# Performance work log

Measured on AMD Instinct MI355X. Metric: run time of the kernel, lower is better.

The kernel has to match this reference:

```python
import jax, jax.numpy as jnp
import numpy as np

B, T, F, H, L = 16384, 24, 7, 8, 4
DENSE = [T * H, 1024, 2048, 4]


def setup_inputs() -> dict:
    key = jax.random.key(0)
    d = {"x": jax.random.normal(jax.random.fold_in(key, 0), (B, T, F), jnp.float32)}
    k = 1
    s = 1.0 / np.sqrt(H)  # torch LSTM init bound
    for l in range(L):
        in_dim = F if l == 0 else H
        for name, shape in [("Wih", (4 * H, in_dim)), ("Whh", (4 * H, H)), ("bih", (4 * H,)), ("bhh", (4 * H,))]:
            d[f"{name}{l}"] = jax.random.uniform(jax.random.fold_in(key, k), shape, jnp.float32, -s, s)
            k += 1
    for i in range(1, len(DENSE)):
        si = 1.0 / np.sqrt(DENSE[i - 1])
        d[f"Wd{i}"] = jax.random.uniform(jax.random.fold_in(key, k), (DENSE[i], DENSE[i - 1]), jnp.float32, -si, si)
        k += 1
        d[f"bd{i}"] = jax.random.uniform(jax.random.fold_in(key, k), (DENSE[i],), jnp.float32, -si, si)
        k += 1
    return d


def _lstm_layer(xs, Wih, Whh, b):
    # xs: [T, B, in] -> ys: [T, B, H]; torch gate order i,f,g,o
    Hn = Whh.shape[1]
    h0 = jnp.zeros((xs.shape[1], Hn), xs.dtype)

    def step(carry, xt):
        h, c = carry
        z = xt @ Wih.T + h @ Whh.T + b  # [B, 4H]
        i, f, g, o = jnp.split(z, 4, axis=-1)
        c = jax.nn.sigmoid(f) * c + jax.nn.sigmoid(i) * jnp.tanh(g)
        h = jax.nn.sigmoid(o) * jnp.tanh(c)
        return (h, c), h

    (_, _), ys = jax.lax.scan(step, (h0, h0), xs)
    return ys


def _forward(x, lstm_params, dense_params):
    xs = jnp.transpose(x, (1, 0, 2))  # [T, B, F]
    for (Wih, Whh, bih, bhh) in lstm_params:
        xs = _lstm_layer(xs, Wih, Whh, bih + bhh)
    out = jnp.transpose(xs, (1, 0, 2)).reshape(x.shape[0], T * H)  # [B, 192]
    (W1, b1), (W2, b2), (W3, b3) = dense_params
    out = jax.nn.relu(out @ W1.T + b1)
    out = jax.nn.relu(out @ W2.T + b2)
    return out @ W3.T + b3  # [B, num_classes]


def reference(x, Wih0, Whh0, bih0, bhh0, Wih1, Whh1, bih1, bhh1, Wih2, Whh2, bih2, bhh2, Wih3, Whh3, bih3, bhh3, Wd1, bd1, Wd2, bd2, Wd3, bd3):
    lstm_params = [(Wih0, Whh0, bih0, bhh0), (Wih1, Whh1, bih1, bhh1), (Wih2, Whh2, bih2, bhh2), (Wih3, Whh3, bih3, bhh3)]
    dense_params = [(Wd1, bd1), (Wd2, bd2), (Wd3, bd3)]
    return _forward(x, lstm_params, dense_params)
```

## Files before the change

### kernel.cpp

```cpp
#include <hip/hip_runtime.h>
#include <hip/hip_bf16.h>

typedef __attribute__((ext_vector_type(4))) float f32x4;
typedef __attribute__((ext_vector_type(16))) float f32x16;
typedef __attribute__((ext_vector_type(2))) float f32x2;
typedef __attribute__((ext_vector_type(8))) short bf16x8;

__device__ __forceinline__ ushort f2bf(float f) {
    union { float f; uint u; } v; v.f = f;
    uint u = v.u;
    return (ushort)((u + 0x7fffu + ((u >> 16) & 1u)) >> 16);
}
__device__ __forceinline__ float sigm(float x) {
    return __builtin_amdgcn_rcpf(1.0f + __builtin_amdgcn_exp2f(x * -1.442695040888963f));
}
__device__ __forceinline__ float tanh_(float x) {
    return 2.0f * __builtin_amdgcn_rcpf(1.0f + __builtin_amdgcn_exp2f(x * -2.885390081777927f)) - 1.0f;
}

typedef const __attribute__((address_space(1))) unsigned int ga_u32;
typedef __attribute__((address_space(3))) unsigned int lds_u32;
__device__ __forceinline__ void g2l16(const void* g, void* l) {
    __builtin_amdgcn_global_load_lds((ga_u32*)(unsigned long long)g,
                                     (lds_u32*)(unsigned int)(unsigned long long)l,
                                     16, 0, 0);
}

struct LstmW {
    const float* wih[4];
    const float* whh[4];
    const float* bih[4];
    const float* bhh[4];
};

__device__ __forceinline__ void gates8p(const f32x2 w01[8], const f32x2 w23[8],
                                        const float xv8[8], f32x2& a01, f32x2& a23) {
#pragma unroll
    for (int k = 0; k < 8; ++k) {
        f32x2 xv = {xv8[k], xv8[k]};
        a01 += w01[k] * xv;
        a23 += w23[k] * xv;
    }
}
__device__ __forceinline__ void cellup(f32x2 a01, f32x2 a23, float& h, float& c) {
    c = sigm(a01.y) * c + sigm(a01.x) * tanh_(a23.x);
    h = sigm(a23.y) * tanh_(c);
}
__device__ __forceinline__ void ld8(const float* p, float v[8]) {
    float4 a = *(const float4*)p;
    float4 b = *(const float4*)(p + 4);
    v[0] = a.x; v[1] = a.y; v[2] = a.z; v[3] = a.w;
    v[4] = b.x; v[5] = b.y; v[6] = b.z; v[7] = b.w;
}

__global__ __launch_bounds__(256) void pre_kernel(const float* __restrict__ x, LstmW p,
                                                  ushort* __restrict__ Y,
                                                  const float* __restrict__ W1,
                                                  const float* __restrict__ W2,
                                                  ushort* __restrict__ W1b,
                                                  ushort* __restrict__ W2b,
                                                  const float* __restrict__ b3,
                                                  float* __restrict__ out) {
    __shared__ float xs[32 * 168];
    __shared__ float hb[32 * 200];

    const int tid = threadIdx.x;
    if (blockIdx.x >= 512) {
        const int tg = (blockIdx.x - 512) * 256 + tid;
        if (tg < 16384) {
            float4 bv = {b3[0], b3[1], b3[2], b3[3]};
            ((float4*)out)[tg] = bv;
        }
#pragma unroll
        for (int s = 0; s < 4; ++s) {
            int i = tg + s * 143360;
            const float4* src; ushort4* dst; int off;
            if (i < 49152) { src = (const float4*)W1; dst = (ushort4*)W1b; off = i; }
            else { src = (const float4*)W2; dst = (ushort4*)W2b; off = i - 49152; }
            float4 v = src[off];
            ushort4 r; r.x = f2bf(v.x); r.y = f2bf(v.y); r.z = f2bf(v.z); r.w = f2bf(v.w);
            dst[off] = r;
        }
        return;
    }

    const int e0 = blockIdx.x * 32;
    {
        const float4* s = (const float4*)(x + (size_t)e0 * 168);
        float4* d = (float4*)xs;
        for (int i = tid; i < 1344; i += 256) d[i] = s[i];
    }
    __syncthreads();

    const int el = tid >> 3, j = tid & 7;
    float* hr = hb + el * 200;
    const float* xr = xs + el * 168;

    f32x2 wx01[8], wx23[8], wh01[8], wh23[8], b01, b23;

    {
        const float* Wih = p.wih[0];
        const float* Whh = p.whh[0];
#pragma unroll
        for (int k = 0; k < 7; ++k) {
            wx01[k] = {Wih[(0 + j) * 7 + k], Wih[(8 + j) * 7 + k]};
            wx23[k] = {Wih[(16 + j) * 7 + k], Wih[(24 + j) * 7 + k]};
        }
#pragma unroll
        for (int k = 0; k < 8; ++k) {
            wh01[k] = {Whh[(0 + j) * 8 + k], Whh[(8 + j) * 8 + k]};
            wh23[k] = {Whh[(16 + j) * 8 + k], Whh[(24 + j) * 8 + k]};
        }
        b01 = {p.bih[0][j] + p.bhh[0][j], p.bih[0][8 + j] + p.bhh[0][8 + j]};
        b23 = {p.bih[0][16 + j] + p.bhh[0][16 + j], p.bih[0][24 + j] + p.bhh[0][24 + j]};

        float h = 0.f, c = 0.f;
        {
            f32x2 a01 = b01, a23 = b23;
#pragma unroll
            for (int k = 0; k < 7; ++k) {
                f32x2 xv = {xr[k], xr[k]};
                a01 += wx01[k] * xv; a23 += wx23[k] * xv;
            }
            cellup(a01, a23, h, c);
            hr[j] = h;
        }
        for (int t = 1; t < 24; ++t) {
            f32x2 a01 = b01, a23 = b23;
#pragma unroll
            for (int k = 0; k < 7; ++k) {
                f32x2 xv = {xr[t * 7 + k], xr[t * 7 + k]};
                a01 += wx01[k] * xv; a23 += wx23[k] * xv;
            }
            float hp[8]; ld8(&hr[(t - 1) * 8], hp);
            gates8p(wh01, wh23, hp, a01, a23);
            cellup(a01, a23, h, c);
            hr[t * 8 + j] = h;
        }
    }

#pragma unroll
    for (int l = 1; l < 4; ++l) {
        const float* Wih = p.wih[l];
        const float* Whh = p.whh[l];
#pragma unroll
        for (int k = 0; k < 8; ++k) {
            wx01[k] = {Wih[(0 + j) * 8 + k], Wih[(8 + j) * 8 + k]};
            wx23[k] = {Wih[(16 + j) * 8 + k], Wih[(24 + j) * 8 + k]};
            wh01[k] = {Whh[(0 + j) * 8 + k], Whh[(8 + j) * 8 + k]};
            wh23[k] = {Whh[(16 + j) * 8 + k], Whh[(24 + j) * 8 + k]};
        }
        b01 = {p.bih[l][j] + p.bhh[l][j], p.bih[l][8 + j] + p.bhh[l][8 + j]};
        b23 = {p.bih[l][16 + j] + p.bhh[l][16 + j], p.bih[l][24 + j] + p.bhh[l][24 + j]};

        float h = 0.f, c = 0.f;
        {
            float xin[8]; ld8(&hr[0], xin);
            f32x2 a01 = b01, a23 = b23;
            gates8p(wx01, wx23, xin, a01, a23);
            cellup(a01, a23, h, c);
            hr[j] = h;
            if (l == 3) Y[((size_t)(e0 + el) * 24) * 8 + j] = f2bf(h);
        }
        for (int t = 1; t < 24; ++t) {
            float xin[8]; ld8(&hr[t * 8], xin);
            float hp[8];  ld8(&hr[(t - 1) * 8], hp);
            f32x2 a01 = b01, a23 = b23;
            gates8p(wx01, wx23, xin, a01, a23);
            gates8p(wh01, wh23, hp, a01, a23);
            cellup(a01, a23, h, c);
            hr[t * 8 + j] = h;
            if (l == 3) Y[((size_t)(e0 + el) * 24 + t) * 8 + j] = f2bf(h);
        }
    }
}

template <int KDIM>
__device__ __forceinline__ void gemm_body(const ushort* __restrict__ A,
                                          const ushort* __restrict__ W,
                                          const float* __restrict__ bias,
                                          ushort* __restrict__ Hout, int N) {
    __shared__ alignas(16) ushort smem[16384];
    ushort* As = smem;
    ushort* Ws = smem + 8192;

    const int tid = threadIdx.x;
    const int m0 = blockIdx.x * 128;
    const int n0 = blockIdx.y * 128;
    const int lane = tid & 63;
    const int wv = tid >> 6;
    const int wm = (wv & 1) * 64;
    const int wn = (wv >> 1) * 64;
    const int l31 = lane & 31;
    const int kh = lane >> 5;

    const int lrow = lane >> 3;
    const int lchunk = (lane & 7) ^ lrow;
    const ushort* Ag = A + (size_t)(m0 + wv * 32 + lrow) * KDIM + lchunk * 8;
    const ushort* Wg = W + (size_t)(n0 + wv * 32 + lrow) * KDIM + lchunk * 8;
    ushort* Ald = As + wv * 2048;
    ushort* Wld = Ws + wv * 2048;

    const int r7 = l31 & 7;
    const int arow0 = (wm + l31) * 64;
    const int brow0 = (wn + l31) * 64;

    f32x16 acc[2][2];
#pragma unroll
    for (int mi = 0; mi < 2; ++mi)
#pragma unroll
        for (int ni = 0; ni < 2; ++ni)
#pragma unroll
            for (int r = 0; r < 16; ++r) acc[mi][ni][r] = 0.f;

    for (int k0 = 0; k0 < KDIM; k0 += 64) {
#pragma unroll
        for (int c = 0; c < 4; ++c)
            g2l16(Ag + (size_t)c * 8 * KDIM + k0, Ald + c * 512);
#pragma unroll
        for (int c = 0; c < 4; ++c)
            g2l16(Wg + (size_t)c * 8 * KDIM + k0, Wld + c * 512);
        __syncthreads();

#pragma unroll
        for (int ks = 0; ks < 4; ++ks) {
            const int ck = ((ks * 2 + kh) ^ r7) * 8;
            bf16x8 afr[2], bfr[2];
#pragma unroll
            for (int mi = 0; mi < 2; ++mi)
                afr[mi] = *(const bf16x8*)&As[arow0 + mi * 2048 + ck];
#pragma unroll
            for (int ni = 0; ni < 2; ++ni)
                bfr[ni] = *(const bf16x8*)&Ws[brow0 + ni * 2048 + ck];
#pragma unroll
            for (int mi = 0; mi < 2; ++mi)
#pragma unroll
                for (int ni = 0; ni < 2; ++ni)
                    acc[mi][ni] = __builtin_amdgcn_mfma_f32_32x32x16_bf16(afr[mi], bfr[ni],
                                                                         acc[mi][ni], 0, 0, 0);
        }
        __syncthreads();
    }

#pragma unroll
    for (int ni = 0; ni < 2; ++ni) {
        const int col = n0 + wn + ni * 32 + l31;
        const float b = bias[col];
#pragma unroll
        for (int mi = 0; mi < 2; ++mi)
#pragma unroll
            for (int r = 0; r < 16; ++r) {
                const int row = m0 + wm + mi * 32 + (r & 3) + 8 * (r >> 2) + 4 * kh;
                Hout[(size_t)row * N + col] = f2bf(fmaxf(acc[mi][ni][r] + b, 0.f));
            }
    }
}

__global__ __launch_bounds__(256, 4) void gemm1_kernel(const ushort* __restrict__ A,
                                                       const ushort* __restrict__ W,
                                                       const float* __restrict__ bias,
                                                       ushort* __restrict__ Hout, int N) {
    gemm_body<192>(A, W, bias, Hout, N);
}

template <int OFFB>
__device__ __forceinline__ bf16x8 dsr(unsigned a) {
    bf16x8 r;
    asm volatile("ds_read_b128 %0, %1 offset:%2"
                 : "=v"(r) : "v"(a), "i"(OFFB));
    return r;
}
template <int QA, int QB, int KS>
__device__ __forceinline__ void mma_sub(f32x4 acc[8][4], const bf16x8 afr[8],
                                        const bf16x8 br[4]) {
#pragma unroll
    for (int mi = 0; mi < 4; ++mi)
#pragma unroll
        for (int ni = 0; ni < 2; ++ni)
            acc[QA * 4 + mi][QB * 2 + ni] = __builtin_amdgcn_mfma_f32_16x16x32_bf16(
                afr[mi * 2 + KS], br[ni * 2 + KS], acc[QA * 4 + mi][QB * 2 + ni],
                0, 0, 0);
}

#define SBAR()  __builtin_amdgcn_s_barrier()
#define SCHED0() __builtin_amdgcn_sched_barrier(0)
#define LGKM(N) do { asm volatile("s_waitcnt lgkmcnt(" #N ")"); SCHED0(); } while (0)
#define VMC(N)  do { asm volatile("s_waitcnt vmcnt(" #N ")" ::: "memory"); } while (0)
#define PRIO1() __builtin_amdgcn_s_setprio(1)
#define PRIO0() do { __builtin_amdgcn_s_setprio(0); SCHED0(); } while (0)

__global__ __launch_bounds__(512) void gemm2_kernel(const ushort* __restrict__ A,
                                                    const ushort* __restrict__ W,
                                                    const float* __restrict__ bias,
                                                    const float* __restrict__ W3,
                                                    float* __restrict__ outf) {
    __shared__ alignas(16) ushort smem[65536];
    __shared__ alignas(16) float w3s[1040];

    const int tid = threadIdx.x;
    const int wg = ((int)blockIdx.x & 7) * 64 + ((int)blockIdx.x >> 3);
    const int m0 = (wg >> 3) << 8;
    const int n0 = (wg & 7) << 8;

    const int lane = tid & 63;
    const int wv = tid >> 6;

    const int lrow = tid >> 3;
    const int lc8 = ((tid & 7) ^ (lrow & 7)) << 3;
    const ushort* Ag = A + (size_t)(m0 + lrow) * 1024 + lc8;
    const ushort* Bg = W + (size_t)(n0 + lrow) * 1024 + lc8;
    ushort* const sA0 = smem;
    ushort* const sB0 = smem + 16384;
    ushort* const sA1 = smem + 32768;
    ushort* const sB1 = smem + 49152;
    const int srow64 = (wv << 3) * 64;

    const int l15 = lane & 15, kq = lane >> 4, r7 = l15 & 7;
    const int wM = wv >> 2, wN = wv & 3;
    const unsigned sbase = (unsigned)(unsigned long long)&smem[0];
    const unsigned pc0B = (unsigned)((kq ^ r7) << 4);
    const unsigned pc1B = pc0B ^ 64u;
    const unsigned aRowB = (unsigned)((wM * 128 + l15) * 128);
    const unsigned bRowB = (unsigned)((wN * 64 + l15) * 128);
    const unsigned aA0p0 = sbase + aRowB + pc0B;
    const unsigned aA0p1 = sbase + aRowB + pc1B;
    const unsigned aA1p0 = aA0p0 + 65536u;
    const unsigned aA1p1 = aA0p1 + 65536u;
    const unsigned bB0p0 = sbase + 32768u + bRowB + pc0B;
    const unsigned bB0p1 = sbase + 32768u + bRowB + pc1B;
    const unsigned bB1p0 = bB0p0 + 65536u;
    const unsigned bB1p1 = bB0p1 + 65536u;

    auto stA = [&](int buf, int h, int kt) {
        ushort* b = buf ? sA1 : sA0;
#pragma unroll
        for (int c = 0; c < 2; ++c)
            g2l16(Ag + (size_t)(h * 128 + c * 64) * 1024 + kt * 64,
                  b + (h * 128 + c * 64) * 64 + srow64);
    };
    auto stB = [&](int buf, int h, int kt) {
        ushort* b = buf ? sB1 : sB0;
#pragma unroll
        for (int c = 0; c < 2; ++c)
            g2l16(Bg + (size_t)(h * 128 + c * 64) * 1024 + kt * 64,
                  b + (h * 128 + c * 64) * 64 + srow64);
    };

    f32x4 acc[8][4];
#pragma unroll
    for (int i = 0; i < 8; ++i)
#pragma unroll
        for (int j = 0; j < 4; ++j)
#pragma unroll
            for (int r = 0; r < 4; ++r) acc[i][j][r] = 0.f;

#pragma unroll
    for (int i = 0; i < 2; ++i) {
        int idx = tid + i * 512;
        w3s[(idx >> 8) * 260 + (idx & 255)] = W3[(size_t)(idx >> 8) * 2048 + n0 + (idx & 255)];
    }
    float bias4[4];
#pragma unroll
    for (int ni = 0; ni < 4; ++ni) bias4[ni] = bias[n0 + wN * 64 + ni * 16 + l15];

    stA(0, 0, 0); stA(0, 1, 0); stB(0, 0, 0); stB(0, 1, 0);
    stB(1, 0, 1); stB(1, 1, 1); stA(1, 0, 1);
    asm volatile("s_waitcnt lgkmcnt(0)");
    VMC(6);
    SBAR(); SCHED0();

    bf16x8 afr[8], b0r[4], b1r[4];
    afr[0] = dsr<0>(aA0p0);    afr[2] = dsr<2048>(aA0p0);
    afr[4] = dsr<4096>(aA0p0); afr[6] = dsr<6144>(aA0p0);
    b0r[0] = dsr<0>(bB0p0);    b0r[2] = dsr<2048>(bB0p0);

#pragma unroll 1
    for (int it = 0; it < 8; ++it) {
        const int k1 = 2 * it + 1, k2 = 2 * it + 2, k3 = 2 * it + 3;
        const bool nl = (it < 7);
        SBAR(); SCHED0();
        afr[1] = dsr<0>(aA0p1);    afr[3] = dsr<2048>(aA0p1);
        afr[5] = dsr<4096>(aA0p1); afr[7] = dsr<6144>(aA0p1);
        b0r[1] = dsr<0>(bB0p1);    b0r[3] = dsr<2048>(bB0p1);
        stA(1, 1, k1);
        LGKM(6); PRIO1(); mma_sub<0, 0, 0>(acc, afr, b0r); PRIO0();
        b1r[0] = dsr<4096>(bB0p0); b1r[2] = dsr<6144>(bB0p0);
        LGKM(2); PRIO1(); mma_sub<0, 0, 1>(acc, afr, b0r); PRIO0();
        SBAR(); SCHED0();
        b1r[1] = dsr<4096>(bB0p1); b1r[3] = dsr<6144>(bB0p1);
        LGKM(2); PRIO1(); mma_sub<0, 1, 0>(acc, afr, b1r); PRIO0();
        afr[0] = dsr<8192>(aA0p0);  afr[2] = dsr<10240>(aA0p0);
        afr[4] = dsr<12288>(aA0p0); afr[6] = dsr<14336>(aA0p0);
        LGKM(4); PRIO1(); mma_sub<0, 1, 1>(acc, afr, b1r); PRIO0();
        SBAR(); SCHED0();
        afr[1] = dsr<8192>(aA0p1);  afr[3] = dsr<10240>(aA0p1);
        afr[5] = dsr<12288>(aA0p1); afr[7] = dsr<14336>(aA0p1);
        if (nl) stB(0, 0, k2);
        LGKM(4); PRIO1(); mma_sub<1, 1, 0>(acc, afr, b1r); PRIO0();
        LGKM(0); PRIO1(); mma_sub<1, 1, 1>(acc, afr, b1r); PRIO0();
        if (nl) { VMC(2); } else { VMC(0); }
        SBAR(); SCHED0();
        if (nl) { stB(0, 1, k2); stA(0, 0, k2); }
        PRIO1(); mma_sub<1, 0, 0>(acc, afr, b0r); PRIO0();
        afr[0] = dsr<8192>(aA1p0);  afr[2] = dsr<10240>(aA1p0);
        afr[4] = dsr<12288>(aA1p0); afr[6] = dsr<14336>(aA1p0);
        b0r[0] = dsr<0>(bB1p0);     b0r[2] = dsr<2048>(bB1p0);
        PRIO1(); mma_sub<1, 0, 1>(acc, afr, b0r); PRIO0();
        SBAR(); SCHED0();
        afr[1] = dsr<8192>(aA1p1);  afr[3] = dsr<10240>(aA1p1);
        afr[5] = dsr<12288>(aA1p1); afr[7] = dsr<14336>(aA1p1);
        b0r[1] = dsr<0>(bB1p1);     b0r[3] = dsr<2048>(bB1p1);
        if (nl) stA(0, 1, k2);
        LGKM(6); PRIO1(); mma_sub<1, 0, 0>(acc, afr, b0r); PRIO0();
        b1r[0] = dsr<4096>(bB1p0); b1r[2] = dsr<6144>(bB1p0);
        LGKM(2); PRIO1(); mma_sub<1, 0, 1>(acc, afr, b0r); PRIO0();
        SBAR(); SCHED0();
        b1r[1] = dsr<4096>(bB1p1); b1r[3] = dsr<6144>(bB1p1);
        LGKM(2); PRIO1(); mma_sub<1, 1, 0>(acc, afr, b1r); PRIO0();
        afr[0] = dsr<0>(aA1p0);    afr[2] = dsr<2048>(aA1p0);
        afr[4] = dsr<4096>(aA1p0); afr[6] = dsr<6144>(aA1p0);
        LGKM(4); PRIO1(); mma_sub<1, 1, 1>(acc, afr, b1r); PRIO0();
        SBAR(); SCHED0();
        afr[1] = dsr<0>(aA1p1);    afr[3] = dsr<2048>(aA1p1);
        afr[5] = dsr<4096>(aA1p1); afr[7] = dsr<6144>(aA1p1);
        if (nl) stB(1, 0, k3);
        LGKM(4); PRIO1(); mma_sub<0, 1, 0>(acc, afr, b1r); PRIO0();
        LGKM(0); PRIO1(); mma_sub<0, 1, 1>(acc, afr, b1r); PRIO0();
        if (nl) { VMC(2); }
        SBAR(); SCHED0();
        if (nl) { stB(1, 1, k3); stA(1, 0, k3); }
        PRIO1(); mma_sub<0, 0, 0>(acc, afr, b0r); PRIO0();
        if (nl) {
            afr[0] = dsr<0>(aA0p0);    afr[2] = dsr<2048>(aA0p0);
            afr[4] = dsr<4096>(aA0p0); afr[6] = dsr<6144>(aA0p0);
            b0r[0] = dsr<0>(bB0p0);    b0r[2] = dsr<2048>(bB0p0);
        }
        PRIO1(); mma_sub<0, 0, 1>(acc, afr, b0r); PRIO0();
    }

    float* Cs = (float*)smem;
    const int drow = tid >> 3;
    const int j8 = tid & 7;
    __syncthreads();
#pragma unroll
    for (int s = 0; s < 4; ++s) {
        if (wM == (s >> 1)) {
            const int mb = (s & 1) * 4;
#pragma unroll
            for (int mi = 0; mi < 4; ++mi)
#pragma unroll
                for (int ni = 0; ni < 4; ++ni) {
                    f32x4 v = acc[mb + mi][ni];
                    const int cbase = (mi * 16 + kq * 4) * 260 + wN * 64 + ni * 16 + l15;
#pragma unroll
                    for (int r = 0; r < 4; ++r)
                        Cs[cbase + r * 260] = fmaxf(v[r] + bias4[ni], 0.f);
                }
        }
        __syncthreads();
        {
            const float* crow = &Cs[drow * 260 + j8 * 4];
            f32x4 pp = {0.f, 0.f, 0.f, 0.f};
#pragma unroll
            for (int k = 0; k < 8; ++k) {
                f32x4 cv = *(const f32x4*)(crow + k * 32);
#pragma unroll
                for (int q = 0; q < 4; ++q) {
                    f32x4 wv4 = *(const f32x4*)(&w3s[q * 260 + j8 * 4 + k * 32]);
                    pp[q] += cv[0] * wv4[0] + cv[1] * wv4[1] + cv[2] * wv4[2] + cv[3] * wv4[3];
                }
            }
#pragma unroll
            for (int m = 1; m < 8; m <<= 1) {
#pragma unroll
                for (int q = 0; q < 4; ++q) pp[q] += __shfl_xor(pp[q], m);
            }
            const float pv = (j8 == 0) ? pp[0] : (j8 == 1) ? pp[1]
                           : (j8 == 2) ? pp[2] : pp[3];
            if (j8 < 4)
                atomicAdd(&outf[(size_t)(m0 + s * 64 + drow) * 4 + j8], pv);
        }
        __syncthreads();
    }
}

extern "C" void kernel_launch(void* const* d_in, const int* in_sizes, int n_in,
                              void* d_out, int out_size, void* d_ws, size_t ws_size,
                              hipStream_t stream) {
    const float* x = (const float*)d_in[0];
    LstmW w;
    for (int l = 0; l < 4; ++l) {
        w.wih[l] = (const float*)d_in[1 + 4 * l];
        w.whh[l] = (const float*)d_in[2 + 4 * l];
        w.bih[l] = (const float*)d_in[3 + 4 * l];
        w.bhh[l] = (const float*)d_in[4 + 4 * l];
    }
    const float* Wd1 = (const float*)d_in[17];
    const float* bd1 = (const float*)d_in[18];
    const float* Wd2 = (const float*)d_in[19];
    const float* bd2 = (const float*)d_in[20];
    const float* Wd3 = (const float*)d_in[21];
    const float* bd3 = (const float*)d_in[22];
    float* out = (float*)d_out;

    ushort* Y   = (ushort*)d_ws;
    ushort* H1  = (ushort*)((char*)d_ws + 6291456);
    ushort* W1b = (ushort*)((char*)d_ws + 39845888);
    ushort* W2b = (ushort*)((char*)d_ws + 40239104);

    pre_kernel<<<1072, 256, 0, stream>>>(x, w, Y, Wd1, Wd2, W1b, W2b, bd3, out);
    gemm1_kernel<<<dim3(128, 8), 256, 0, stream>>>(Y, W1b, bd1, H1, 1024);
    gemm2_kernel<<<512, 512, 0, stream>>>(H1, W2b, bd2, Wd3, out);
}
```

Measured before the change: 211.3 us.

## Exchange LSTM hidden state via ds_swizzle and split weight conversion into own kernel

The recurrent hidden-state vector is now broadcast among the 8 lanes of each sequence element with ds_swizzle instead of being reloaded from LDS each timestep. The last layer no longer writes hidden states to LDS. The weight bf16 conversion and output bias initialization move from extra blocks of the LSTM kernel into a separate launch. This shortens the serial dependency chain per step at the cost of one more kernel launch.

```diff
diff --git a/kernel.cpp b/kernel.cpp
--- a/kernel.cpp
+++ b/kernel.cpp
@@ -52,38 +52,47 @@
     v[0] = a.x; v[1] = a.y; v[2] = a.z; v[3] = a.w;
     v[4] = b.x; v[5] = b.y; v[6] = b.z; v[7] = b.w;
 }
-
-__global__ __launch_bounds__(256) void pre_kernel(const float* __restrict__ x, LstmW p,
-                                                  ushort* __restrict__ Y,
-                                                  const float* __restrict__ W1,
-                                                  const float* __restrict__ W2,
-                                                  ushort* __restrict__ W1b,
-                                                  ushort* __restrict__ W2b,
-                                                  const float* __restrict__ b3,
-                                                  float* __restrict__ out) {
+__device__ __forceinline__ void hswz(float h, float hp[8]) {
+    const int hi = __float_as_int(h);
+    hp[0] = __int_as_float(__builtin_amdgcn_ds_swizzle(hi, 0x18));
+    hp[1] = __int_as_float(__builtin_amdgcn_ds_swizzle(hi, 0x38));
+    hp[2] = __int_as_float(__builtin_amdgcn_ds_swizzle(hi, 0x58));
+    hp[3] = __int_as_float(__builtin_amdgcn_ds_swizzle(hi, 0x78));
+    hp[4] = __int_as_float(__builtin_amdgcn_ds_swizzle(hi, 0x98));
+    hp[5] = __int_as_float(__builtin_amdgcn_ds_swizzle(hi, 0xB8));
+    hp[6] = __int_as_float(__builtin_amdgcn_ds_swizzle(hi, 0xD8));
+    hp[7] = __int_as_float(__builtin_amdgcn_ds_swizzle(hi, 0xF8));
+}
+
+__global__ __launch_bounds__(256) void wcvt_kernel(const float* __restrict__ W1,
+                                                   const float* __restrict__ W2,
+                                                   ushort* __restrict__ W1b,
+                                                   ushort* __restrict__ W2b,
+                                                   const float* __restrict__ b3,
+                                                   float* __restrict__ out) {
+    const int tg = blockIdx.x * 256 + threadIdx.x;
+    if (tg < 16384) {
+        float4 bv = {b3[0], b3[1], b3[2], b3[3]};
+        ((float4*)out)[tg] = bv;
+    }
+#pragma unroll
+    for (int s = 0; s < 4; ++s) {
+        int i = tg + s * 143360;
+        const float4* src; ushort4* dst; int off;
+        if (i < 49152) { src = (const float4*)W1; dst = (ushort4*)W1b; off = i; }
+        else { src = (const float4*)W2; dst = (ushort4*)W2b; off = i - 49152; }
+        float4 v = src[off];
+        ushort4 r; r.x = f2bf(v.x); r.y = f2bf(v.y); r.z = f2bf(v.z); r.w = f2bf(v.w);
+        dst[off] = r;
+    }
+}
+
+__global__ __launch_bounds__(256) void lstm_kernel(const float* __restrict__ x, LstmW p,
+                                                   ushort* __restrict__ Y) {
     __shared__ float xs[32 * 168];
     __shared__ float hb[32 * 200];
 
     const int tid = threadIdx.x;
-    if (blockIdx.x >= 512) {
-        const int tg = (blockIdx.x - 512) * 256 + tid;
-        if (tg < 16384) {
-            float4 bv = {b3[0], b3[1], b3[2], b3[3]};
-            ((float4*)out)[tg] = bv;
-        }
-#pragma unroll
-        for (int s = 0; s < 4; ++s) {
-            int i = tg + s * 143360;
-            const float4* src; ushort4* dst; int off;
-            if (i < 49152) { src = (const float4*)W1; dst = (ushort4*)W1b; off = i; }
-            else { src = (const float4*)W2; dst = (ushort4*)W2b; off = i - 49152; }
-            float4 v = src[off];
-            ushort4 r; r.x = f2bf(v.x); r.y = f2bf(v.y); r.z = f2bf(v.z); r.w = f2bf(v.w);
-            dst[off] = r;
-        }
-        return;
-    }
-
     const int e0 = blockIdx.x * 32;
     {
         const float4* s = (const float4*)(x + (size_t)e0 * 168);
@@ -126,13 +135,13 @@
             hr[j] = h;
         }
         for (int t = 1; t < 24; ++t) {
+            float hp[8]; hswz(h, hp);
             f32x2 a01 = b01, a23 = b23;
 #pragma unroll
             for (int k = 0; k < 7; ++k) {
                 f32x2 xv = {xr[t * 7 + k], xr[t * 7 + k]};
                 a01 += wx01[k] * xv; a23 += wx23[k] * xv;
             }
-            float hp[8]; ld8(&hr[(t - 1) * 8], hp);
             gates8p(wh01, wh23, hp, a01, a23);
             cellup(a01, a23, h, c);
             hr[t * 8 + j] = h;
@@ -159,18 +168,18 @@
             f32x2 a01 = b01, a23 = b23;
             gates8p(wx01, wx23, xin, a01, a23);
             cellup(a01, a23, h, c);
-            hr[j] = h;
-            if (l == 3) Y[((size_t)(e0 + el) * 24) * 8 + j] = f2bf(h);
+            if (l < 3) hr[j] = h;
+            else Y[((size_t)(e0 + el) * 24) * 8 + j] = f2bf(h);
         }
         for (int t = 1; t < 24; ++t) {
             float xin[8]; ld8(&hr[t * 8], xin);
-            float hp[8];  ld8(&hr[(t - 1) * 8], hp);
+            float hp[8];  hswz(h, hp);
             f32x2 a01 = b01, a23 = b23;
             gates8p(wx01, wx23, xin, a01, a23);
             gates8p(wh01, wh23, hp, a01, a23);
             cellup(a01, a23, h, c);
-            hr[t * 8 + j] = h;
-            if (l == 3) Y[((size_t)(e0 + el) * 24 + t) * 8 + j] = f2bf(h);
+            if (l < 3) hr[t * 8 + j] = h;
+            else Y[((size_t)(e0 + el) * 24 + t) * 8 + j] = f2bf(h);
         }
     }
 }
@@ -508,7 +517,8 @@
     ushort* W1b = (ushort*)((char*)d_ws + 39845888);
     ushort* W2b = (ushort*)((char*)d_ws + 40239104);
 
-    pre_kernel<<<1072, 256, 0, stream>>>(x, w, Y, Wd1, Wd2, W1b, W2b, bd3, out);
+    wcvt_kernel<<<560, 256, 0, stream>>>(Wd1, Wd2, W1b, W2b, bd3, out);
+    lstm_kernel<<<512, 256, 0, stream>>>(x, w, Y);
     gemm1_kernel<<<dim3(128, 8), 256, 0, stream>>>(Y, W1b, bd1, H1, 1024);
     gemm2_kernel<<<512, 512, 0, stream>>>(H1, W2b, bd2, Wd3, out);
 }
```

New measurement: 223.7 us. 1.06x slower.

## Pipeline the four LSTM layers across wavefronts with a diagonal time schedule

Applied to the files above, without the earlier changes.

Each block now handles 8 sequences instead of 32. Each of its four wavefronts owns one LSTM layer and runs it on a skewed schedule: layer g processes timestep tau-g, and layers pass hidden states through a small double-buffered LDS area. This cuts the per-block serial chain from 96 cell updates to 27 barrier-separated steps, and the smaller LDS footprint allows four times as many blocks. The cost is a block-wide barrier every step and the idle wavefronts during pipeline fill and drain.

```diff
diff --git a/kernel.cpp b/kernel.cpp
--- a/kernel.cpp
+++ b/kernel.cpp
@@ -61,12 +61,9 @@
                                                   ushort* __restrict__ W2b,
                                                   const float* __restrict__ b3,
                                                   float* __restrict__ out) {
-    __shared__ float xs[32 * 168];
-    __shared__ float hb[32 * 200];
-
     const int tid = threadIdx.x;
-    if (blockIdx.x >= 512) {
-        const int tg = (blockIdx.x - 512) * 256 + tid;
+    if (blockIdx.x >= 2048) {
+        const int tg = (blockIdx.x - 2048) * 256 + tid;
         if (tg < 16384) {
             float4 bv = {b3[0], b3[1], b3[2], b3[3]};
             ((float4*)out)[tg] = bv;
@@ -84,93 +81,70 @@
         return;
     }
 
-    const int e0 = blockIdx.x * 32;
+    __shared__ float xs[8 * 168];
+    __shared__ float hx[2 * 4 * 8 * 8];
+
+    const int e0 = blockIdx.x * 8;
     {
         const float4* s = (const float4*)(x + (size_t)e0 * 168);
         float4* d = (float4*)xs;
-        for (int i = tid; i < 1344; i += 256) d[i] = s[i];
-    }
-    __syncthreads();
-
-    const int el = tid >> 3, j = tid & 7;
-    float* hr = hb + el * 200;
-    const float* xr = xs + el * 168;
+        for (int i = tid; i < 336; i += 256) d[i] = s[i];
+    }
+
+    const int g = tid >> 6;
+    const int e = (tid >> 3) & 7;
+    const int j = tid & 7;
+    const float* xr = xs + e * 168;
 
     f32x2 wx01[8], wx23[8], wh01[8], wh23[8], b01, b23;
-
     {
-        const float* Wih = p.wih[0];
-        const float* Whh = p.whh[0];
-#pragma unroll
-        for (int k = 0; k < 7; ++k) {
-            wx01[k] = {Wih[(0 + j) * 7 + k], Wih[(8 + j) * 7 + k]};
-            wx23[k] = {Wih[(16 + j) * 7 + k], Wih[(24 + j) * 7 + k]};
+        const float* Wih = p.wih[g];
+        const float* Whh = p.whh[g];
+        if (g == 0) {
+#pragma unroll
+            for (int k = 0; k < 7; ++k) {
+                wx01[k] = {Wih[(0 + j) * 7 + k], Wih[(8 + j) * 7 + k]};
+                wx23[k] = {Wih[(16 + j) * 7 + k], Wih[(24 + j) * 7 + k]};
+            }
+        } else {
+#pragma unroll
+            for (int k = 0; k < 8; ++k) {
+                wx01[k] = {Wih[(0 + j) * 8 + k], Wih[(8 + j) * 8 + k]};
+                wx23[k] = {Wih[(16 + j) * 8 + k], Wih[(24 + j) * 8 + k]};
+            }
         }
 #pragma unroll
         for (int k = 0; k < 8; ++k) {
             wh01[k] = {Whh[(0 + j) * 8 + k], Whh[(8 + j) * 8 + k]};
             wh23[k] = {Whh[(16 + j) * 8 + k], Whh[(24 + j) * 8 + k]};
         }
-        b01 = {p.bih[0][j] + p.bhh[0][j], p.bih[0][8 + j] + p.bhh[0][8 + j]};
-        b23 = {p.bih[0][16 + j] + p.bhh[0][16 + j], p.bih[0][24 + j] + p.bhh[0][24 + j]};
-
-        float h = 0.f, c = 0.f;
-        {
+        b01 = {p.bih[g][j] + p.bhh[g][j], p.bih[g][8 + j] + p.bhh[g][8 + j]};
+        b23 = {p.bih[g][16 + j] + p.bhh[g][16 + j], p.bih[g][24 + j] + p.bhh[g][24 + j]};
+    }
+
+    float h = 0.f, c = 0.f;
+    for (int tau = 0; tau < 27; ++tau) {
+        __syncthreads();
+        const int t = tau - g;
+        if (t >= 0 && t < 24) {
             f32x2 a01 = b01, a23 = b23;
-#pragma unroll
-            for (int k = 0; k < 7; ++k) {
-                f32x2 xv = {xr[k], xr[k]};
-                a01 += wx01[k] * xv; a23 += wx23[k] * xv;
+            if (g == 0) {
+#pragma unroll
+                for (int k = 0; k < 7; ++k) {
+                    f32x2 xv = {xr[t * 7 + k], xr[t * 7 + k]};
+                    a01 += wx01[k] * xv; a23 += wx23[k] * xv;
+                }
+            } else {
+                float xin[8]; ld8(&hx[(((t & 1) << 2) + (g - 1)) * 64 + e * 8], xin);
+                gates8p(wx01, wx23, xin, a01, a23);
+            }
+            if (t > 0) {
+                float hp[8]; ld8(&hx[((((t - 1) & 1) << 2) + g) * 64 + e * 8], hp);
+                gates8p(wh01, wh23, hp, a01, a23);
             }
             cellup(a01, a23, h, c);
-            hr[j] = h;
-        }
-        for (int t = 1; t < 24; ++t) {
-            f32x2 a01 = b01, a23 = b23;
-#pragma unroll
-            for (int k = 0; k < 7; ++k) {
-                f32x2 xv = {xr[t * 7 + k], xr[t * 7 + k]};
-                a01 += wx01[k] * xv; a23 += wx23[k] * xv;
-            }
-            float hp[8]; ld8(&hr[(t - 1) * 8], hp);
-            gates8p(wh01, wh23, hp, a01, a23);
-            cellup(a01, a23, h, c);
-            hr[t * 8 + j] = h;
-        }
-    }
-
-#pragma unroll
-    for (int l = 1; l < 4; ++l) {
-        const float* Wih = p.wih[l];
-        const float* Whh = p.whh[l];
-#pragma unroll
-        for (int k = 0; k < 8; ++k) {
-            wx01[k] = {Wih[(0 + j) * 8 + k], Wih[(8 + j) * 8 + k]};
-            wx23[k] = {Wih[(16 + j) * 8 + k], Wih[(24 + j) * 8 + k]};
-            wh01[k] = {Whh[(0 + j) * 8 + k], Whh[(8 + j) * 8 + k]};
-            wh23[k] = {Whh[(16 + j) * 8 + k], Whh[(24 + j) * 8 + k]};
-        }
-        b01 = {p.bih[l][j] + p.bhh[l][j], p.bih[l][8 + j] + p.bhh[l][8 + j]};
-        b23 = {p.bih[l][16 + j] + p.bhh[l][16 + j], p.bih[l][24 + j] + p.bhh[l][24 + j]};
-
-        float h = 0.f, c = 0.f;
-        {
-            float xin[8]; ld8(&hr[0], xin);
-            f32x2 a01 = b01, a23 = b23;
-            gates8p(wx01, wx23, xin, a01, a23);
-            cellup(a01, a23, h, c);
-            hr[j] = h;
-            if (l == 3) Y[((size_t)(e0 + el) * 24) * 8 + j] = f2bf(h);
-        }
-        for (int t = 1; t < 24; ++t) {
-            float xin[8]; ld8(&hr[t * 8], xin);
-            float hp[8];  ld8(&hr[(t - 1) * 8], hp);
-            f32x2 a01 = b01, a23 = b23;
-            gates8p(wx01, wx23, xin, a01, a23);
-            gates8p(wh01, wh23, hp, a01, a23);
-            cellup(a01, a23, h, c);
-            hr[t * 8 + j] = h;
-            if (l == 3) Y[((size_t)(e0 + el) * 24 + t) * 8 + j] = f2bf(h);
+            hx[(((t & 1) << 2) + g) * 64 + e * 8 + j] = h;
+            if (g == 3) Y[((size_t)(e0 + e) * 24 + t) * 8 + j] = f2bf(h);
         }
     }
 }
@@ -508,7 +482,7 @@
     ushort* W1b = (ushort*)((char*)d_ws + 39845888);
     ushort* W2b = (ushort*)((char*)d_ws + 40239104);
 
-    pre_kernel<<<1072, 256, 0, stream>>>(x, w, Y, Wd1, Wd2, W1b, W2b, bd3, out);
+    pre_kernel<<<2608, 256, 0, stream>>>(x, w, Y, Wd1, Wd2, W1b, W2b, bd3, out);
     gemm1_kernel<<<dim3(128, 8), 256, 0, stream>>>(Y, W1b, bd1, H1, 1024);
     gemm2_kernel<<<512, 512, 0, stream>>>(H1, W2b, bd2, Wd3, out);
 }
```

Result: slower. 217.4 us (+2.9%).

## Fuse first dense layer GEMM into LSTM kernel epilogue

Applied to the files above, without the earlier changes.

Removes the separate gemm1 kernel and the bf16 Y intermediate. After the LSTM layers finish, each block runs the first dense layer (192->1024) for its 32 rows with 16x16x32 MFMAs. The LSTM output is read from LDS and W1 rows are converted from fp32 global memory to bf16 on the fly. This saves a launch and the round-trip of Y through HBM, but every block now rereads all of W1 in fp32 and the dense work runs at the LSTM kernel's lower occupancy.

```diff
diff --git a/kernel.cpp b/kernel.cpp
--- a/kernel.cpp
+++ b/kernel.cpp
@@ -16,6 +16,15 @@
 }
 __device__ __forceinline__ float tanh_(float x) {
     return 2.0f * __builtin_amdgcn_rcpf(1.0f + __builtin_amdgcn_exp2f(x * -2.885390081777927f)) - 1.0f;
+}
+__device__ __forceinline__ uint pk2(float a, float b) {
+    uint r; asm("v_cvt_pk_bf16_f32 %0, %1, %2" : "=v"(r) : "v"(a), "v"(b)); return r;
+}
+__device__ __forceinline__ bf16x8 pk8(f32x4 lo, f32x4 hi) {
+    union { bf16x8 v; uint u[4]; } r;
+    r.u[0] = pk2(lo[0], lo[1]); r.u[1] = pk2(lo[2], lo[3]);
+    r.u[2] = pk2(hi[0], hi[1]); r.u[3] = pk2(hi[2], hi[3]);
+    return r.v;
 }
 
 typedef const __attribute__((address_space(1))) unsigned int ga_u32;
@@ -54,16 +63,13 @@
 }
 
 __global__ __launch_bounds__(256) void pre_kernel(const float* __restrict__ x, LstmW p,
-                                                  ushort* __restrict__ Y,
                                                   const float* __restrict__ W1,
+                                                  const float* __restrict__ b1,
                                                   const float* __restrict__ W2,
-                                                  ushort* __restrict__ W1b,
                                                   ushort* __restrict__ W2b,
                                                   const float* __restrict__ b3,
-                                                  float* __restrict__ out) {
-    __shared__ float xs[32 * 168];
-    __shared__ float hb[32 * 200];
-
+                                                  float* __restrict__ out,
+                                                  ushort* __restrict__ H1) {
     const int tid = threadIdx.x;
     if (blockIdx.x >= 512) {
         const int tg = (blockIdx.x - 512) * 256 + tid;
@@ -73,16 +79,16 @@
         }
 #pragma unroll
         for (int s = 0; s < 4; ++s) {
-            int i = tg + s * 143360;
-            const float4* src; ushort4* dst; int off;
-            if (i < 49152) { src = (const float4*)W1; dst = (ushort4*)W1b; off = i; }
-            else { src = (const float4*)W2; dst = (ushort4*)W2b; off = i - 49152; }
-            float4 v = src[off];
+            int i = tg + s * 131072;
+            float4 v = ((const float4*)W2)[i];
             ushort4 r; r.x = f2bf(v.x); r.y = f2bf(v.y); r.z = f2bf(v.z); r.w = f2bf(v.w);
-            dst[off] = r;
+            ((ushort4*)W2b)[i] = r;
         }
         return;
     }
+
+    __shared__ float xs[32 * 168];
+    __shared__ float hb[32 * 200];
 
     const int e0 = blockIdx.x * 32;
     {
@@ -160,7 +166,6 @@
             gates8p(wx01, wx23, xin, a01, a23);
             cellup(a01, a23, h, c);
             hr[j] = h;
-            if (l == 3) Y[((size_t)(e0 + el) * 24) * 8 + j] = f2bf(h);
         }
         for (int t = 1; t < 24; ++t) {
             float xin[8]; ld8(&hr[t * 8], xin);
@@ -170,97 +175,51 @@
             gates8p(wh01, wh23, hp, a01, a23);
             cellup(a01, a23, h, c);
             hr[t * 8 + j] = h;
-            if (l == 3) Y[((size_t)(e0 + el) * 24 + t) * 8 + j] = f2bf(h);
-        }
-    }
-}
-
-template <int KDIM>
-__device__ __forceinline__ void gemm_body(const ushort* __restrict__ A,
-                                          const ushort* __restrict__ W,
-                                          const float* __restrict__ bias,
-                                          ushort* __restrict__ Hout, int N) {
-    __shared__ alignas(16) ushort smem[16384];
-    ushort* As = smem;
-    ushort* Ws = smem + 8192;
-
-    const int tid = threadIdx.x;
-    const int m0 = blockIdx.x * 128;
-    const int n0 = blockIdx.y * 128;
-    const int lane = tid & 63;
-    const int wv = tid >> 6;
-    const int wm = (wv & 1) * 64;
-    const int wn = (wv >> 1) * 64;
-    const int l31 = lane & 31;
-    const int kh = lane >> 5;
-
-    const int lrow = lane >> 3;
-    const int lchunk = (lane & 7) ^ lrow;
-    const ushort* Ag = A + (size_t)(m0 + wv * 32 + lrow) * KDIM + lchunk * 8;
-    const ushort* Wg = W + (size_t)(n0 + wv * 32 + lrow) * KDIM + lchunk * 8;
-    ushort* Ald = As + wv * 2048;
-    ushort* Wld = Ws + wv * 2048;
-
-    const int r7 = l31 & 7;
-    const int arow0 = (wm + l31) * 64;
-    const int brow0 = (wn + l31) * 64;
-
-    f32x16 acc[2][2];
-#pragma unroll
-    for (int mi = 0; mi < 2; ++mi)
-#pragma unroll
-        for (int ni = 0; ni < 2; ++ni)
-#pragma unroll
-            for (int r = 0; r < 16; ++r) acc[mi][ni][r] = 0.f;
-
-    for (int k0 = 0; k0 < KDIM; k0 += 64) {
-#pragma unroll
-        for (int c = 0; c < 4; ++c)
-            g2l16(Ag + (size_t)c * 8 * KDIM + k0, Ald + c * 512);
-#pragma unroll
-        for (int c = 0; c < 4; ++c)
-            g2l16(Wg + (size_t)c * 8 * KDIM + k0, Wld + c * 512);
-        __syncthreads();
-
-#pragma unroll
-        for (int ks = 0; ks < 4; ++ks) {
-            const int ck = ((ks * 2 + kh) ^ r7) * 8;
-            bf16x8 afr[2], bfr[2];
-#pragma unroll
-            for (int mi = 0; mi < 2; ++mi)
-                afr[mi] = *(const bf16x8*)&As[arow0 + mi * 2048 + ck];
-#pragma unroll
-            for (int ni = 0; ni < 2; ++ni)
-                bfr[ni] = *(const bf16x8*)&Ws[brow0 + ni * 2048 + ck];
-#pragma unroll
-            for (int mi = 0; mi < 2; ++mi)
-#pragma unroll
-                for (int ni = 0; ni < 2; ++ni)
-                    acc[mi][ni] = __builtin_amdgcn_mfma_f32_32x32x16_bf16(afr[mi], bfr[ni],
-                                                                         acc[mi][ni], 0, 0, 0);
-        }
-        __syncthreads();
-    }
-
-#pragma unroll
-    for (int ni = 0; ni < 2; ++ni) {
-        const int col = n0 + wn + ni * 32 + l31;
-        const float b = bias[col];
-#pragma unroll
-        for (int mi = 0; mi < 2; ++mi)
-#pragma unroll
-            for (int r = 0; r < 16; ++r) {
-                const int row = m0 + wm + mi * 32 + (r & 3) + 8 * (r >> 2) + 4 * kh;
-                Hout[(size_t)row * N + col] = f2bf(fmaxf(acc[mi][ni][r] + b, 0.f));
-            }
-    }
-}
-
-__global__ __launch_bounds__(256, 4) void gemm1_kernel(const ushort* __restrict__ A,
-                                                       const ushort* __restrict__ W,
-                                                       const float* __restrict__ bias,
-                                                       ushort* __restrict__ Hout, int N) {
-    gemm_body<192>(A, W, bias, Hout, N);
+        }
+    }
+
+    __syncthreads();
+    {
+        const int lane = tid & 63;
+        const int wv = tid >> 6;
+        const int l15 = lane & 15, kq = lane >> 4;
+        const int nw0 = wv * 256;
+
+        bf16x8 abf[2][6];
+#pragma unroll
+        for (int mf = 0; mf < 2; ++mf)
+#pragma unroll
+            for (int ks = 0; ks < 6; ++ks) {
+                const float* ap = hb + (mf * 16 + l15) * 200 + ks * 32 + kq * 8;
+                f32x4 lo = *(const f32x4*)ap;
+                f32x4 hi = *(const f32x4*)(ap + 4);
+                abf[mf][ks] = pk8(lo, hi);
+            }
+#pragma unroll
+        for (int nf = 0; nf < 16; ++nf) {
+            const int col = nw0 + nf * 16 + l15;
+            const float* wrow = W1 + (size_t)col * 192;
+            bf16x8 bbf[6];
+#pragma unroll
+            for (int ks = 0; ks < 6; ++ks) {
+                f32x4 lo = *(const f32x4*)(wrow + ks * 32 + kq * 8);
+                f32x4 hi = *(const f32x4*)(wrow + ks * 32 + kq * 8 + 4);
+                bbf[ks] = pk8(lo, hi);
+            }
+            f32x4 a0 = {0.f, 0.f, 0.f, 0.f}, a1 = {0.f, 0.f, 0.f, 0.f};
+#pragma unroll
+            for (int ks = 0; ks < 6; ++ks) {
+                a0 = __builtin_amdgcn_mfma_f32_16x16x32_bf16(abf[0][ks], bbf[ks], a0, 0, 0, 0);
+                a1 = __builtin_amdgcn_mfma_f32_16x16x32_bf16(abf[1][ks], bbf[ks], a1, 0, 0, 0);
+            }
+            const float bv = b1[col];
+#pragma unroll
+            for (int r = 0; r < 4; ++r) {
+                H1[(size_t)(e0 + kq * 4 + r) * 1024 + col]      = f2bf(fmaxf(a0[r] + bv, 0.f));
+                H1[(size_t)(e0 + 16 + kq * 4 + r) * 1024 + col] = f2bf(fmaxf(a1[r] + bv, 0.f));
+            }
+        }
+    }
 }
 
 template <int OFFB>
@@ -503,12 +462,9 @@
     const float* bd3 = (const float*)d_in[22];
     float* out = (float*)d_out;
 
-    ushort* Y   = (ushort*)d_ws;
     ushort* H1  = (ushort*)((char*)d_ws + 6291456);
-    ushort* W1b = (ushort*)((char*)d_ws + 39845888);
     ushort* W2b = (ushort*)((char*)d_ws + 40239104);
 
-    pre_kernel<<<1072, 256, 0, stream>>>(x, w, Y, Wd1, Wd2, W1b, W2b, bd3, out);
-    gemm1_kernel<<<dim3(128, 8), 256, 0, stream>>>(Y, W1b, bd1, H1, 1024);
+    pre_kernel<<<1024, 256, 0, stream>>>(x, w, Wd1, bd1, Wd2, W2b, bd3, out, H1);
     gemm2_kernel<<<512, 512, 0, stream>>>(H1, W2b, bd2, Wd3, out);
 }
```

After: 225.7 us. 6.8% more time.
